# Optimization experiments

Measured on AMD Instinct MI355X. Metric: run time of the kernel, lower is better.

## Reference

```python
import jax, jax.numpy as jnp
import numpy as np

KD, KH, KW = 3, 3, 3
C = 64

def setup_inputs() -> dict:
    key = jax.random.key(0)
    kx, kw = jax.random.split(key)
    x = jax.random.normal(kx, (4, 16, 112, 112, C), dtype=jnp.float32)
    # One 3x3x3 filter per channel; DHWIO layout with I=in_per_group=1, O=C
    w = jax.random.normal(kw, (KD, KH, KW, 1, C), dtype=jnp.float32) * 0.1
    return {"x": x, "w": w}

def reference(x, w) -> jnp.ndarray:
    # Depthwise 3D conv: feature_group_count=C makes each output channel the
    # conv of the matching input channel with its own [3,3,3] kernel, which is
    # exactly the per-channel Conv3D(filters=1) loop + concat in the original.
    return jax.lax.conv_general_dilated(
        x, w,
        window_strides=(1, 1, 1),
        padding="SAME",
        dimension_numbers=("NDHWC", "DHWIO", "NDHWC"),
        feature_group_count=C,
    )
```

## Files before the change

### kernel.cpp

```cpp
#include <hip/hip_runtime.h>

#define N_ 4
#define D_ 16
#define H_ 112
#define W_ 112
#define C_ 64

#define DO_ 2
#define HO_ 2
#define DT_ (D_ / DO_)
#define HTILES (H_ / HO_)
#define WAVES_PER_BLOCK 4
#define HGROUPS (HTILES / WAVES_PER_BLOCK)
#define WSPLIT 2
#define WHALF (W_ / WSPLIT)

__global__ __launch_bounds__(256)
void dwconv3d_kernel(const float* __restrict__ x,
                     const float* __restrict__ wgt,
                     float* __restrict__ out) {
    int b = blockIdx.x;
    const int wh = b % WSPLIT; b /= WSPLIT;
    const int hg = b % HGROUPS; b /= HGROUPS;
    const int dt = b % DT_;     b /= DT_;
    const int n  = b;

    const int lane = threadIdx.x & 63;
    const int wid  = threadIdx.x >> 6;
    const int c    = lane;

    const int d0 = dt * DO_;
    const int h0 = (hg * WAVES_PER_BLOCK + wid) * HO_;
    const int w0 = wh * WHALF;

    float wt[3][3][3];
#pragma unroll
    for (int kd = 0; kd < 3; ++kd)
#pragma unroll
      for (int kh = 0; kh < 3; ++kh)
#pragma unroll
        for (int kw = 0; kw < 3; ++kw)
          wt[kd][kh][kw] = wgt[((kd * 3 + kh) * 3 + kw) * C_ + c];

    const float* px[4][4];
    float msk[4][4];
#pragma unroll
    for (int dr = 0; dr < 4; ++dr) {
      int d = d0 - 1 + dr;
      bool dv = (d >= 0) && (d < D_);
      int dc = d < 0 ? 0 : (d > D_ - 1 ? D_ - 1 : d);
#pragma unroll
      for (int hr = 0; hr < 4; ++hr) {
        int h = h0 - 1 + hr;
        bool hv = (h >= 0) && (h < H_);
        int hc = h < 0 ? 0 : (h > H_ - 1 ? H_ - 1 : h);
        msk[dr][hr] = (dv && hv) ? 1.0f : 0.0f;
        px[dr][hr] = x + (size_t)((n * D_ + dc) * H_ + hc) * W_ * C_ + c;
      }
    }

    float win[3][4][4];

    if (w0 == 0) {
#pragma unroll
      for (int dr = 0; dr < 4; ++dr)
#pragma unroll
        for (int hr = 0; hr < 4; ++hr)
          win[0][dr][hr] = 0.0f;
    } else {
#pragma unroll
      for (int dr = 0; dr < 4; ++dr)
#pragma unroll
        for (int hr = 0; hr < 4; ++hr)
          win[0][dr][hr] = msk[dr][hr] * px[dr][hr][(size_t)(w0 - 1) * C_];
    }
#pragma unroll
    for (int dr = 0; dr < 4; ++dr)
#pragma unroll
      for (int hr = 0; hr < 4; ++hr) {
        win[1][dr][hr] = msk[dr][hr] * px[dr][hr][(size_t)(w0)     * C_];
        win[2][dr][hr] = msk[dr][hr] * px[dr][hr][(size_t)(w0 + 1) * C_];
      }

    float* po[2][2];
#pragma unroll
    for (int od = 0; od < 2; ++od)
#pragma unroll
      for (int oh = 0; oh < 2; ++oh)
        po[od][oh] = out + ((size_t)((n * D_ + d0 + od) * H_ + (h0 + oh)) * W_ + w0) * C_ + c;

#pragma unroll
    for (int dr = 0; dr < 4; ++dr)
#pragma unroll
      for (int hr = 0; hr < 4; ++hr)
        px[dr][hr] += (size_t)(w0 + 2) * C_;

#pragma unroll 4
    for (int w = w0; w < w0 + WHALF; ++w) {
      float acc[2][2];
#pragma unroll
      for (int od = 0; od < 2; ++od)
#pragma unroll
        for (int oh = 0; oh < 2; ++oh) {
          float a = 0.0f;
#pragma unroll
          for (int kw = 0; kw < 3; ++kw)
#pragma unroll
            for (int kd = 0; kd < 3; ++kd)
#pragma unroll
              for (int kh = 0; kh < 3; ++kh)
                a += win[kw][od + kd][oh + kh] * wt[kd][kh][kw];
          acc[od][oh] = a;
        }
#pragma unroll
      for (int od = 0; od < 2; ++od)
#pragma unroll
        for (int oh = 0; oh < 2; ++oh) {
          *po[od][oh] = acc[od][oh];
          po[od][oh] += C_;
        }
#pragma unroll
      for (int dr = 0; dr < 4; ++dr)
#pragma unroll
        for (int hr = 0; hr < 4; ++hr) {
          win[0][dr][hr] = win[1][dr][hr];
          win[1][dr][hr] = win[2][dr][hr];
        }
      if (w + 2 < W_) {
#pragma unroll
        for (int dr = 0; dr < 4; ++dr)
#pragma unroll
          for (int hr = 0; hr < 4; ++hr) {
            win[2][dr][hr] = msk[dr][hr] * px[dr][hr][0];
            px[dr][hr] += C_;
          }
      } else {
#pragma unroll
        for (int dr = 0; dr < 4; ++dr)
#pragma unroll
          for (int hr = 0; hr < 4; ++hr)
            win[2][dr][hr] = 0.0f;
      }
    }
}

extern "C" void kernel_launch(void* const* d_in, const int* in_sizes, int n_in,
                              void* d_out, int out_size, void* d_ws, size_t ws_size,
                              hipStream_t stream) {
    const float* x   = (const float*)d_in[0];
    const float* wgt = (const float*)d_in[1];
    float* out = (float*)d_out;

    dim3 grid(N_ * DT_ * HGROUPS * WSPLIT);
    dim3 block(256);
    dwconv3d_kernel<<<grid, block, 0, stream>>>(x, wgt, out);
}
```

Baseline: 389.6 us.

## Replace boundary mask multiplies with zero-page pointers and split W into four chunks

Out-of-range depth/height rows now point at a small zeroed workspace page with a zero stride, so the per-load mask multiply is gone and invalid rows hit one cached line. The W dimension is split into four chunks instead of two, doubling the grid to raise parallelism. A tiny extra kernel launch zeroes the page each call, and shorter chunks raise the relative cost of halo loads and prologue setup.

```diff
diff --git a/kernel.cpp b/kernel.cpp
--- a/kernel.cpp
+++ b/kernel.cpp
@@ -12,15 +12,18 @@
 #define HTILES (H_ / HO_)
 #define WAVES_PER_BLOCK 4
 #define HGROUPS (HTILES / WAVES_PER_BLOCK)
-#define WSPLIT 2
-#define WHALF (W_ / WSPLIT)
+#define WSPLIT 4
+#define WCHUNK (W_ / WSPLIT)
+
+__global__ void zero_page_kernel(float* zp) { zp[threadIdx.x] = 0.0f; }
 
 __global__ __launch_bounds__(256)
 void dwconv3d_kernel(const float* __restrict__ x,
                      const float* __restrict__ wgt,
-                     float* __restrict__ out) {
+                     float* __restrict__ out,
+                     const float* __restrict__ zp) {
     int b = blockIdx.x;
-    const int wh = b % WSPLIT; b /= WSPLIT;
+    const int wh = b % WSPLIT;  b /= WSPLIT;
     const int hg = b % HGROUPS; b /= HGROUPS;
     const int dt = b % DT_;     b /= DT_;
     const int n  = b;
@@ -31,7 +34,7 @@
 
     const int d0 = dt * DO_;
     const int h0 = (hg * WAVES_PER_BLOCK + wid) * HO_;
-    const int w0 = wh * WHALF;
+    const int w0 = wh * WCHUNK;
 
     float wt[3][3][3];
 #pragma unroll
@@ -42,20 +45,23 @@
         for (int kw = 0; kw < 3; ++kw)
           wt[kd][kh][kw] = wgt[((kd * 3 + kh) * 3 + kw) * C_ + c];
 
-    const float* px[4][4];
-    float msk[4][4];
+    const float* q[4][4];
+    int step[4][4];
 #pragma unroll
     for (int dr = 0; dr < 4; ++dr) {
       int d = d0 - 1 + dr;
-      bool dv = (d >= 0) && (d < D_);
-      int dc = d < 0 ? 0 : (d > D_ - 1 ? D_ - 1 : d);
 #pragma unroll
       for (int hr = 0; hr < 4; ++hr) {
         int h = h0 - 1 + hr;
-        bool hv = (h >= 0) && (h < H_);
-        int hc = h < 0 ? 0 : (h > H_ - 1 ? H_ - 1 : h);
-        msk[dr][hr] = (dv && hv) ? 1.0f : 0.0f;
-        px[dr][hr] = x + (size_t)((n * D_ + dc) * H_ + hc) * W_ * C_ + c;
+        bool valid = (d >= 0) && (d < D_) && (h >= 0) && (h < H_);
+        if (valid) {
+          q[dr][hr] = x + (size_t)((n * D_ + d) * H_ + h) * W_ * C_
+                        + (size_t)w0 * C_ + c;
+          step[dr][hr] = C_;
+        } else {
+          q[dr][hr] = zp + c;
+          step[dr][hr] = 0;
+        }
       }
     }
 
@@ -72,14 +78,15 @@
       for (int dr = 0; dr < 4; ++dr)
 #pragma unroll
         for (int hr = 0; hr < 4; ++hr)
-          win[0][dr][hr] = msk[dr][hr] * px[dr][hr][(size_t)(w0 - 1) * C_];
+          win[0][dr][hr] = q[dr][hr][-step[dr][hr]];
     }
 #pragma unroll
     for (int dr = 0; dr < 4; ++dr)
 #pragma unroll
       for (int hr = 0; hr < 4; ++hr) {
-        win[1][dr][hr] = msk[dr][hr] * px[dr][hr][(size_t)(w0)     * C_];
-        win[2][dr][hr] = msk[dr][hr] * px[dr][hr][(size_t)(w0 + 1) * C_];
+        win[1][dr][hr] = q[dr][hr][0];
+        win[2][dr][hr] = q[dr][hr][step[dr][hr]];
+        q[dr][hr] += 2 * step[dr][hr];
       }
 
     float* po[2][2];
@@ -89,14 +96,8 @@
       for (int oh = 0; oh < 2; ++oh)
         po[od][oh] = out + ((size_t)((n * D_ + d0 + od) * H_ + (h0 + oh)) * W_ + w0) * C_ + c;
 
-#pragma unroll
-    for (int dr = 0; dr < 4; ++dr)
-#pragma unroll
-      for (int hr = 0; hr < 4; ++hr)
-        px[dr][hr] += (size_t)(w0 + 2) * C_;
-
 #pragma unroll 4
-    for (int w = w0; w < w0 + WHALF; ++w) {
+    for (int w = w0; w < w0 + WCHUNK; ++w) {
       float acc[2][2];
 #pragma unroll
       for (int od = 0; od < 2; ++od)
@@ -131,8 +132,8 @@
         for (int dr = 0; dr < 4; ++dr)
 #pragma unroll
           for (int hr = 0; hr < 4; ++hr) {
-            win[2][dr][hr] = msk[dr][hr] * px[dr][hr][0];
-            px[dr][hr] += C_;
+            win[2][dr][hr] = q[dr][hr][0];
+            q[dr][hr] += step[dr][hr];
           }
       } else {
 #pragma unroll
@@ -150,8 +151,11 @@
     const float* x   = (const float*)d_in[0];
     const float* wgt = (const float*)d_in[1];
     float* out = (float*)d_out;
+    float* zp  = (float*)d_ws;
+
+    zero_page_kernel<<<1, 64, 0, stream>>>(zp);
 
     dim3 grid(N_ * DT_ * HGROUPS * WSPLIT);
     dim3 block(256);
-    dwconv3d_kernel<<<grid, block, 0, stream>>>(x, wgt, out);
+    dwconv3d_kernel<<<grid, block, 0, stream>>>(x, wgt, out, zp);
 }
```

Result: slower. 430.9 us (+10.6%).
